# Optimization experiments

Hardware: AMD Instinct MI355X
Metric: run time of the kernel (lower is better)

The kernel has to match this reference:

```python
import jax, jax.numpy as jnp
import numpy as np

D, H, L, FF, EPS = 3, 3, 12, 2048, 1e-5
B, C, T = 32, 2, 64


def _ln(x, g, b):
    m = jnp.mean(x, -1, keepdims=True)
    v = jnp.mean((x - m) ** 2, -1, keepdims=True)
    return (x - m) / jnp.sqrt(v + EPS) * g + b


def _mha(xq, xkv, w, b, ow, ob):
    # xq: [Tq,B,D], xkv: [S,B,D]; w: [3D,D] packed q/k/v like torch in_proj_weight
    Tq, Bb, _ = xq.shape
    S = xkv.shape[0]
    q = xq @ w[:D].T + b[:D]
    k = xkv @ w[D:2 * D].T + b[D:2 * D]
    v = xkv @ w[2 * D:].T + b[2 * D:]
    dh = D // H  # = 1
    q = q.reshape(Tq, Bb, H, dh)
    k = k.reshape(S, Bb, H, dh)
    v = v.reshape(S, Bb, H, dh)
    scores = jnp.einsum('qbhd,kbhd->bhqk', q, k) * (1.0 / np.sqrt(dh))
    att = jax.nn.softmax(scores, axis=-1)
    o = jnp.einsum('bhqk,kbhd->qbhd', att, v).reshape(Tq, Bb, D)
    return o @ ow.T + ob


def _ffn(x, w1, b1, w2, b2):
    return jax.nn.relu(x @ w1.T + b1) @ w2.T + b2


def _encode(x, p):
    def layer(h, pl):
        aw, ab, aow, aob, g1, b1, g2, b2, f1w, f1b, f2w, f2b = pl
        h = _ln(h + _mha(h, h, aw, ab, aow, aob), g1, b1)
        h = _ln(h + _ffn(h, f1w, f1b, f2w, f2b), g2, b2)
        return h, None
    h, _ = jax.lax.scan(layer, x, p)
    return h


def _decode(tgt, mem, p):
    def layer(h, pl):
        (sw, sb, sow, sob, cw, cb, cow, cob,
         g1, b1, g2, b2, g3, b3, f1w, f1b, f2w, f2b) = pl
        h = _ln(h + _mha(h, h, sw, sb, sow, sob), g1, b1)      # self-attn (no mask, as in source)
        h = _ln(h + _mha(h, mem, cw, cb, cow, cob), g2, b2)    # cross-attn
        h = _ln(h + _ffn(h, f1w, f1b, f2w, f2b), g3, b3)
        return h, None
    h, _ = jax.lax.scan(layer, tgt, p)
    return h


def _forward(src, angle, enc_p, enc_ng, enc_nb, dec_p, dec_ng, dec_nb):
    Bb, _, Tt = src.shape
    a = jnp.broadcast_to(angle.reshape(Bb, 1, 1), (Bb, 1, Tt))
    x = jnp.transpose(jnp.concatenate([src, a], axis=1), (2, 0, 1))  # [T,B,3]
    mem = _ln(_encode(x, enc_p), enc_ng, enc_nb)  # encoder memory is loop-invariant

    def dec(o):
        return _ln(_decode(o, mem, dec_p), dec_ng, dec_nb)

    out = jnp.zeros_like(x).at[0].set(x[0])

    def step(o, t):
        pred = dec(o)
        return o.at[t].set(pred[t]), None

    out, _ = jax.lax.scan(step, out, jnp.arange(1, Tt))
    return jnp.transpose(out, (1, 2, 0))  # [B,3,T]


def setup_inputs() -> dict:
    key = jax.random.key(0)
    it = iter(jax.random.split(key, 40))
    def n(shape, s=0.05):
        return jax.random.normal(next(it), shape, dtype=jnp.float32) * s
    inp = {
        'src': jax.random.normal(next(it), (B, C, T), dtype=jnp.float32),
        'angle': jax.random.normal(next(it), (B,), dtype=jnp.float32),
        'enc_attn_w': n((L, 3 * D, D)), 'enc_attn_b': n((L, 3 * D)),
        'enc_attn_ow': n((L, D, D)), 'enc_attn_ob': n((L, D)),
        'enc_ln1_g': jnp.ones((L, D)), 'enc_ln1_b': jnp.zeros((L, D)),
        'enc_ln2_g': jnp.ones((L, D)), 'enc_ln2_b': jnp.zeros((L, D)),
        'enc_ff1_w': n((L, FF, D)), 'enc_ff1_b': n((L, FF)),
        'enc_ff2_w': n((L, D, FF)), 'enc_ff2_b': n((L, D)),
        'enc_norm_g': jnp.ones((D,)), 'enc_norm_b': jnp.zeros((D,)),
        'dec_sa_w': n((L, 3 * D, D)), 'dec_sa_b': n((L, 3 * D)),
        'dec_sa_ow': n((L, D, D)), 'dec_sa_ob': n((L, D)),
        'dec_ca_w': n((L, 3 * D, D)), 'dec_ca_b': n((L, 3 * D)),
        'dec_ca_ow': n((L, D, D)), 'dec_ca_ob': n((L, D)),
        'dec_ln1_g': jnp.ones((L, D)), 'dec_ln1_b': jnp.zeros((L, D)),
        'dec_ln2_g': jnp.ones((L, D)), 'dec_ln2_b': jnp.zeros((L, D)),
        'dec_ln3_g': jnp.ones((L, D)), 'dec_ln3_b': jnp.zeros((L, D)),
        'dec_ff1_w': n((L, FF, D)), 'dec_ff1_b': n((L, FF)),
        'dec_ff2_w': n((L, D, FF)), 'dec_ff2_b': n((L, D)),
        'dec_norm_g': jnp.ones((D,)), 'dec_norm_b': jnp.zeros((D,)),
    }
    return inp


def reference(src, angle,
              enc_attn_w, enc_attn_b, enc_attn_ow, enc_attn_ob,
              enc_ln1_g, enc_ln1_b, enc_ln2_g, enc_ln2_b,
              enc_ff1_w, enc_ff1_b, enc_ff2_w, enc_ff2_b,
              enc_norm_g, enc_norm_b,
              dec_sa_w, dec_sa_b, dec_sa_ow, dec_sa_ob,
              dec_ca_w, dec_ca_b, dec_ca_ow, dec_ca_ob,
              dec_ln1_g, dec_ln1_b, dec_ln2_g, dec_ln2_b, dec_ln3_g, dec_ln3_b,
              dec_ff1_w, dec_ff1_b, dec_ff2_w, dec_ff2_b,
              dec_norm_g, dec_norm_b):
    enc_p = (enc_attn_w, enc_attn_b, enc_attn_ow, enc_attn_ob,
             enc_ln1_g, enc_ln1_b, enc_ln2_g, enc_ln2_b,
             enc_ff1_w, enc_ff1_b, enc_ff2_w, enc_ff2_b)
    dec_p = (dec_sa_w, dec_sa_b, dec_sa_ow, dec_sa_ob,
             dec_ca_w, dec_ca_b, dec_ca_ow, dec_ca_ob,
             dec_ln1_g, dec_ln1_b, dec_ln2_g, dec_ln2_b, dec_ln3_g, dec_ln3_b,
             dec_ff1_w, dec_ff1_b, dec_ff2_w, dec_ff2_b)
    return _forward(src, angle, enc_p, enc_norm_g, enc_norm_b, dec_p, dec_norm_g, dec_norm_b)
```

## Files before the change

### kernel.cpp

```cpp
#include <hip/hip_runtime.h>

#define DEV static __device__ __forceinline__

typedef _Float16 h2 __attribute__((ext_vector_type(2)));

DEV float fdot2f(h2 a, h2 b, float c) {
#if __has_builtin(__builtin_amdgcn_fdot2)
  return __builtin_amdgcn_fdot2(a, b, c, false);
#else
  return c + (float)a.x * (float)b.x + (float)a.y * (float)b.y;
#endif
}

DEV void ln3(float& a, float& b, float& c, const float* g, const float* bt) {
  float m = (a + b + c) * (1.0f / 3.0f);
  float d0 = a - m, d1 = b - m, d2 = c - m;
  float v = (d0 * d0 + d1 * d1 + d2 * d2) * (1.0f / 3.0f);
  float rs = rsqrtf(v + 1e-5f);
  a = fmaf(d0 * rs, g[0], bt[0]);
  b = fmaf(d1 * rs, g[1], bt[1]);
  c = fmaf(d2 * rs, g[2], bt[2]);
}

DEV unsigned pkh2(float a, float b) {
  h2 v = {(_Float16)a, (_Float16)b};
  return __builtin_bit_cast(unsigned, v);
}

__global__ void __launch_bounds__(256) prepack_kernel(
    const float* ea_w, const float* ea_b, const float* ea_ow, const float* ea_ob,
    const float* el1g, const float* el1b, const float* el2g, const float* el2b,
    const float* ef1w, const float* ef1b, const float* ef2w, const float* ef2b,
    const float* eng, const float* enb,
    const float* dsw, const float* dsb, const float* dsow, const float* dsob,
    const float* dcw, const float* dcb, const float* dcow, const float* dcob,
    const float* dl1g, const float* dl1b, const float* dl2g, const float* dl2b,
    const float* dl3g, const float* dl3b,
    const float* df1w, const float* df1b, const float* df2w, const float* df2b,
    const float* dng, const float* dnb,
    float* ws) {
  const int l = blockIdx.x, tid = threadIdx.x;
  const bool enc = l < 12;
  const int li = enc ? l : l - 12;
  const float* f1w = (enc ? ef1w : df1w) + li * 2048 * 3;
  const float* f1b = (enc ? ef1b : df1b) + li * 2048;
  const float* f2w = (enc ? ef2w : df2w) + li * 3 * 2048;
  uint4* FA4 = (uint4*)ws + (size_t)l * 2048;
  uint4* FB4 = FA4 + 1024;
  for (int jp = tid; jp < 1024; jp += 256) {
    const int j0 = jp * 2, j1 = j0 + 1;
    uint4 A;
    A.x = pkh2(f1w[j0 * 3 + 0], f1w[j1 * 3 + 0]);
    A.y = pkh2(f1w[j0 * 3 + 1], f1w[j1 * 3 + 1]);
    A.z = pkh2(f1w[j0 * 3 + 2], f1w[j1 * 3 + 2]);
    A.w = pkh2(f1b[j0], f1b[j1]);
    FA4[jp] = A;
    uint4 Bv;
    Bv.x = pkh2(f2w[j0], f2w[j1]);
    Bv.y = pkh2(f2w[2048 + j0], f2w[2048 + j1]);
    Bv.z = pkh2(f2w[4096 + j0], f2w[4096 + j1]);
    Bv.w = 0u;
    FB4[jp] = Bv;
  }
  float* S = ws + 196608 + l * 128;
  if (tid == 0) {
    const float* aw = (enc ? ea_w : dsw) + li * 27;
    const float* ab = (enc ? ea_b : dsb) + li * 9;
    const float* aow = (enc ? ea_ow : dsow) + li * 9;
    const float* aob = (enc ? ea_ob : dsob) + li * 3;
    for (int i = 0; i < 27; ++i) S[i] = aw[i];
    for (int i = 0; i < 9; ++i) S[27 + i] = ab[i];
    for (int i = 0; i < 9; ++i) S[36 + i] = aow[i];
    for (int i = 0; i < 3; ++i) S[45 + i] = aob[i];
    const float* p;
    p = (enc ? el1g : dl1g) + li * 3; for (int i = 0; i < 3; ++i) S[48 + i] = p[i];
    p = (enc ? el1b : dl1b) + li * 3; for (int i = 0; i < 3; ++i) S[51 + i] = p[i];
    p = (enc ? el2g : dl2g) + li * 3; for (int i = 0; i < 3; ++i) S[54 + i] = p[i];
    p = (enc ? el2b : dl2b) + li * 3; for (int i = 0; i < 3; ++i) S[57 + i] = p[i];
    p = (enc ? ef2b : df2b) + li * 3; for (int i = 0; i < 3; ++i) S[60 + i] = p[i];
    if (!enc) {
      const float* cw = dcw + li * 27;
      for (int i = 0; i < 9; ++i) {
        S[64 + i] = cw[i];
        S[94 + i] = cw[9 + i];
        S[106 + i] = cw[18 + i];
      }
      const float* cb = dcb + li * 9;
      for (int i = 0; i < 3; ++i) {
        S[73 + i] = cb[i];
        S[103 + i] = cb[3 + i];
        S[115 + i] = cb[6 + i];
      }
      for (int i = 0; i < 9; ++i) S[76 + i] = dcow[li * 9 + i];
      for (int i = 0; i < 3; ++i) S[85 + i] = dcob[li * 3 + i];
      p = dl3g + li * 3; for (int i = 0; i < 3; ++i) S[88 + i] = p[i];
      p = dl3b + li * 3; for (int i = 0; i < 3; ++i) S[91 + i] = p[i];
    }
  }
  if (l == 0 && tid == 1) {
    float* G = ws + 196608 + 24 * 128;
    for (int i = 0; i < 3; ++i) {
      G[i] = eng[i]; G[3 + i] = enb[i];
      G[6 + i] = dng[i]; G[9 + i] = dnb[i];
    }
  }
}

template <int NR>
DEV void ffn_core(const uint4* FA, uint4 pa0, uint4 pc0, uint4 pa1, uint4 pc1,
                  const float (&X0)[4], const float (&X1)[4], const float (&X2)[4],
                  float (&acc)[4][3], int lane) {
  h2 xd0[NR], xd1[NR], xd2[NR];
#pragma unroll
  for (int i = 0; i < NR; ++i) {
    xd0[i] = h2{(_Float16)X0[i], (_Float16)X0[i]};
    xd1[i] = h2{(_Float16)X1[i], (_Float16)X1[i]};
    xd2[i] = h2{(_Float16)X2[i], (_Float16)X2[i]};
  }
#pragma unroll
  for (int i = 0; i < NR; ++i) { acc[i][0] = 0.f; acc[i][1] = 0.f; acc[i][2] = 0.f; }
  const h2 z = {(_Float16)0, (_Float16)0};
  auto step = [&](uint4 a, uint4 c) {
    h2 wa0 = __builtin_bit_cast(h2, a.x), wa1 = __builtin_bit_cast(h2, a.y);
    h2 wa2 = __builtin_bit_cast(h2, a.z), bb = __builtin_bit_cast(h2, a.w);
    h2 wc0 = __builtin_bit_cast(h2, c.x), wc1 = __builtin_bit_cast(h2, c.y);
    h2 wc2 = __builtin_bit_cast(h2, c.z);
#pragma unroll
    for (int i = 0; i < NR; ++i) {
      h2 t = wa0 * xd0[i] + wa1 * xd1[i] + wa2 * xd2[i] + bb;
      t = __builtin_elementwise_max(t, z);
      acc[i][0] = fdot2f(wc0, t, acc[i][0]);
      acc[i][1] = fdot2f(wc1, t, acc[i][1]);
      acc[i][2] = fdot2f(wc2, t, acc[i][2]);
    }
  };
  step(pa0, pc0);
  step(pa1, pc1);
#pragma unroll 4
  for (int kk = 2; kk < 16; ++kk) {
    const int jp = lane + (kk << 6);
    step(FA[jp], FA[1024 + jp]);
  }
#pragma unroll
  for (int m = 1; m < 64; m <<= 1) {
#pragma unroll
    for (int i = 0; i < NR; ++i) {
      acc[i][0] += __shfl_xor(acc[i][0], m, 64);
      acc[i][1] += __shfl_xor(acc[i][1], m, 64);
      acc[i][2] += __shfl_xor(acc[i][2], m, 64);
    }
  }
}

template <bool DEC>
DEV void run_layer(const float* sm, const float* smn, const uint4* FA,
                   const float (*ckv)[8],
                   float (*h)[5], float (*hln)[5], float* kvq,
                   float (*p1)[25], float (*p2)[25],
                   float (*o_s)[5], const float* glob,
                   int R, int t, bool do_p1, bool from_os, bool wpred,
                   int wave, int lane, int tid) {
  uint4 pa0 = FA[lane], pc0 = FA[1024 + lane];
  uint4 pa1 = FA[64 + lane], pc1 = FA[1024 + 64 + lane];
  if (do_p1) {
    const int r = tid >> 4, o = tid & 15;
    if (r < R && o <= 9) {
      float x0, x1, x2;
      if (DEC && from_os) {
        const bool real = r < t;
        x0 = real ? o_s[r][0] : 0.f;
        x1 = real ? o_s[r][1] : 0.f;
        x2 = real ? o_s[r][2] : 0.f;
      } else {
        x0 = h[r][0]; x1 = h[r][1]; x2 = h[r][2];
      }
      if (o < 9) {
        float v = fmaf(sm[o * 3], x0,
                  fmaf(sm[o * 3 + 1], x1, fmaf(sm[o * 3 + 2], x2, sm[27 + o])));
        kvq[r * 13 + o + o / 3] = v;
      } else {
        kvq[r * 13 + 7] = (DEC && r == R - 1 && t > 0) ? (float)(64 - t) : 1.0f;
        if (DEC && from_os) { h[r][0] = x0; h[r][1] = x1; h[r][2] = x2; }
      }
    }
    if (DEC && o == 9 && r >= R) kvq[r * 13 + 7] = 0.f;
    __syncthreads();
  }
  if (wave < 12) {
    const int hd = wave % 3, c = wave / 3;
    const int p0 = c * 16;
    float den = 0.f, num = 0.f;
    if (p0 < R) {
      const float q = kvq[lane * 13 + hd] * 1.44269504f;
#pragma unroll
      for (int pp = 0; pp < 16; ++pp) {
        const int p = p0 + pp;
        float e = exp2f(q * kvq[p * 13 + 4 + hd]);
        if (DEC) e *= kvq[p * 13 + 7];
        den += e;
        num = fmaf(e, kvq[p * 13 + 8 + hd], num);
      }
    }
    p1[lane][2 * wave] = den;
    p1[lane][2 * wave + 1] = num;
  }
  __syncthreads();
  if (DEC) {
    if (wave < 12) {
      const int r = lane, hd = wave % 3, c = wave / 3;
      float d0 = p1[r][0] + p1[r][6] + p1[r][12] + p1[r][18];
      float n0 = p1[r][1] + p1[r][7] + p1[r][13] + p1[r][19];
      float d1 = p1[r][2] + p1[r][8] + p1[r][14] + p1[r][20];
      float n1 = p1[r][3] + p1[r][9] + p1[r][15] + p1[r][21];
      float d2 = p1[r][4] + p1[r][10] + p1[r][16] + p1[r][22];
      float n2 = p1[r][5] + p1[r][11] + p1[r][17] + p1[r][23];
      float oh0 = __fdividef(n0, d0), oh1 = __fdividef(n1, d1), oh2 = __fdividef(n2, d2);
      float a0 = fmaf(sm[36], oh0, fmaf(sm[37], oh1, fmaf(sm[38], oh2, sm[45]))) + h[r][0];
      float a1 = fmaf(sm[39], oh0, fmaf(sm[40], oh1, fmaf(sm[41], oh2, sm[46]))) + h[r][1];
      float a2 = fmaf(sm[42], oh0, fmaf(sm[43], oh1, fmaf(sm[44], oh2, sm[47]))) + h[r][2];
      ln3(a0, a1, a2, sm + 48, sm + 51);
      if (wave == 0 && r < R) { hln[r][0] = a0; hln[r][1] = a1; hln[r][2] = a2; }
      float q = fmaf(sm[64 + hd * 3], a0,
                fmaf(sm[64 + hd * 3 + 1], a1,
                fmaf(sm[64 + hd * 3 + 2], a2, sm[73 + hd]))) * 1.44269504f;
      const int p0 = c * 16;
      float den = 0.f, num = 0.f;
#pragma unroll
      for (int pp = 0; pp < 16; ++pp) {
        const int p = p0 + pp;
        float e = exp2f(q * ckv[p][hd]);
        den += e;
        num = fmaf(e, ckv[p][3 + hd], num);
      }
      p2[r][2 * wave] = den;
      p2[r][2 * wave + 1] = num;
    }
    __syncthreads();
  }
  {
    const int nr = (wave < R) ? (1 + (R - 1 - wave) / 16) : 0;
    if (nr > 0) {
      const float(*pp)[25] = DEC ? p2 : p1;
      const float* ow = DEC ? sm + 76 : sm + 36;
      const float* ob = DEC ? sm + 85 : sm + 45;
      const float* lg = DEC ? sm + 54 : sm + 48;
      const float* lb = DEC ? sm + 57 : sm + 51;
      float X0[4], X1[4], X2[4];
#pragma unroll
      for (int i = 0; i < 4; ++i) {
        X0[i] = 0.f; X1[i] = 0.f; X2[i] = 0.f;
        if (i < nr) {
          const int rc = wave + 16 * i;
          float d0 = pp[rc][0] + pp[rc][6] + pp[rc][12] + pp[rc][18];
          float n0 = pp[rc][1] + pp[rc][7] + pp[rc][13] + pp[rc][19];
          float d1 = pp[rc][2] + pp[rc][8] + pp[rc][14] + pp[rc][20];
          float n1 = pp[rc][3] + pp[rc][9] + pp[rc][15] + pp[rc][21];
          float d2 = pp[rc][4] + pp[rc][10] + pp[rc][16] + pp[rc][22];
          float n2 = pp[rc][5] + pp[rc][11] + pp[rc][17] + pp[rc][23];
          float oh0 = __fdividef(n0, d0), oh1 = __fdividef(n1, d1), oh2 = __fdividef(n2, d2);
          float hr0, hr1, hr2;
          if (DEC) { hr0 = hln[rc][0]; hr1 = hln[rc][1]; hr2 = hln[rc][2]; }
          else     { hr0 = h[rc][0];   hr1 = h[rc][1];   hr2 = h[rc][2]; }
          float a0 = fmaf(ow[0], oh0, fmaf(ow[1], oh1, fmaf(ow[2], oh2, ob[0]))) + hr0;
          float a1 = fmaf(ow[3], oh0, fmaf(ow[4], oh1, fmaf(ow[5], oh2, ob[1]))) + hr1;
          float a2 = fmaf(ow[6], oh0, fmaf(ow[7], oh1, fmaf(ow[8], oh2, ob[2]))) + hr2;
          ln3(a0, a1, a2, lg, lb);
          X0[i] = a0; X1[i] = a1; X2[i] = a2;
        }
      }
      float acc[4][3];
      switch (nr) {
        case 1: ffn_core<1>(FA, pa0, pc0, pa1, pc1, X0, X1, X2, acc, lane); break;
        case 2: ffn_core<2>(FA, pa0, pc0, pa1, pc1, X0, X1, X2, acc, lane); break;
        case 3: ffn_core<3>(FA, pa0, pc0, pa1, pc1, X0, X1, X2, acc, lane); break;
        default: ffn_core<4>(FA, pa0, pc0, pa1, pc1, X0, X1, X2, acc, lane); break;
      }
      const float* fg = DEC ? sm + 88 : sm + 54;
      const float* fb = DEC ? sm + 91 : sm + 57;
#pragma unroll
      for (int i = 0; i < 4; ++i) {
        if (i < nr) {
          const int r = wave + 16 * i;
          float y0 = acc[i][0] + sm[60] + X0[i];
          float y1 = acc[i][1] + sm[61] + X1[i];
          float y2 = acc[i][2] + sm[62] + X2[i];
          ln3(y0, y1, y2, fg, fb);
          if (lane == 0) {
            h[r][0] = y0; h[r][1] = y1; h[r][2] = y2;
            if (DEC && wpred && r == R - 1) {
              float z0 = y0, z1 = y1, z2 = y2;
              ln3(z0, z1, z2, glob + 6, glob + 9);
              o_s[t][0] = z0; o_s[t][1] = z1; o_s[t][2] = z2;
            }
          }
          if (smn && lane >= 9 * i && lane < 9 * i + 9) {
            const int o = lane - 9 * i;
            kvq[r * 13 + o + o / 3] =
                fmaf(smn[o * 3], y0,
                fmaf(smn[o * 3 + 1], y1, fmaf(smn[o * 3 + 2], y2, smn[27 + o])));
          }
        }
      }
    }
    __syncthreads();
  }
}

__global__ void __launch_bounds__(1024) tf_kernel(const float* src, const float* angle,
                                                  const float* ws, float* out) {
  __shared__ float small_s[24][128];
  __shared__ float glob[16];
  __shared__ float h[64][5];
  __shared__ float hln[64][5];
  __shared__ float kvq[64 * 13];
  __shared__ float p1[64][25];
  __shared__ float p2[64][25];
  __shared__ float o_s[64][5];
  __shared__ float ckcv[12][64][8];
  const int b = blockIdx.x;
  const int tid = threadIdx.x, wave = tid >> 6, lane = tid & 63;
  const uint4* FABg = (const uint4*)ws;
  const float* SM = ws + 196608;
  const float* GB = SM + 24 * 128;
  for (int i = tid; i < 24 * 128; i += 1024) ((float*)small_s)[i] = SM[i];
  if (tid < 16) glob[tid] = GB[tid];
  if (tid < 64) {
    float x0 = src[b * 128 + tid];
    float x1 = src[b * 128 + 64 + tid];
    float x2 = angle[b];
    h[tid][0] = x0; h[tid][1] = x1; h[tid][2] = x2;
    o_s[tid][0] = (tid == 0) ? x0 : 0.f;
    o_s[tid][1] = (tid == 0) ? x1 : 0.f;
    o_s[tid][2] = (tid == 0) ? x2 : 0.f;
  }
  __syncthreads();
  for (int l = 0; l < 12; ++l)
    run_layer<false>(small_s[l], (l < 11) ? small_s[l + 1] : nullptr,
                     FABg + (size_t)l * 2048, nullptr,
                     h, hln, kvq, p1, p2, o_s, glob,
                     64, 0, l == 0, false, false, wave, lane, tid);
  if (tid < 64) {
    float a = h[tid][0], bb = h[tid][1], c = h[tid][2];
    ln3(a, bb, c, glob + 0, glob + 3);
    h[tid][0] = a; h[tid][1] = bb; h[tid][2] = c;
  }
  __syncthreads();
  if (wave < 12) {
    const float* sm = small_s[12 + wave];
    float m0 = h[lane][0], m1 = h[lane][1], m2 = h[lane][2];
    float k0 = fmaf(sm[94], m0, fmaf(sm[95], m1, fmaf(sm[96], m2, sm[103])));
    float k1 = fmaf(sm[97], m0, fmaf(sm[98], m1, fmaf(sm[99], m2, sm[104])));
    float k2 = fmaf(sm[100], m0, fmaf(sm[101], m1, fmaf(sm[102], m2, sm[105])));
    float v0 = fmaf(sm[106], m0, fmaf(sm[107], m1, fmaf(sm[108], m2, sm[115])));
    float v1 = fmaf(sm[109], m0, fmaf(sm[110], m1, fmaf(sm[111], m2, sm[116])));
    float v2 = fmaf(sm[112], m0, fmaf(sm[113], m1, fmaf(sm[114], m2, sm[117])));
    ckcv[wave][lane][0] = k0; ckcv[wave][lane][1] = k1; ckcv[wave][lane][2] = k2;
    ckcv[wave][lane][3] = v0; ckcv[wave][lane][4] = v1; ckcv[wave][lane][5] = v2;
  }
  __syncthreads();
  for (int t = 1; t < 64; ++t) {
    const int R = t + 1;
    for (int li = 0; li < 12; ++li)
      run_layer<true>(small_s[12 + li], (li < 11) ? small_s[12 + li + 1] : nullptr,
                      FABg + (size_t)(12 + li) * 2048,
                      (const float(*)[8])ckcv[li],
                      h, hln, kvq, p1, p2, o_s, glob, R, t,
                      li == 0, li == 0, li == 11,
                      wave, lane, tid);
  }
  if (tid < 192) {
    int d = tid / 64, tt = tid % 64;
    out[b * 192 + tid] = o_s[tt][d];
  }
}

extern "C" void kernel_launch(void* const* d_in, const int* in_sizes, int n_in,
                              void* d_out, int out_size, void* d_ws, size_t ws_size,
                              hipStream_t stream) {
  (void)in_sizes; (void)n_in; (void)out_size; (void)ws_size;
  float* ws = (float*)d_ws;
  prepack_kernel<<<24, 256, 0, stream>>>(
      (const float*)d_in[2], (const float*)d_in[3], (const float*)d_in[4], (const float*)d_in[5],
      (const float*)d_in[6], (const float*)d_in[7], (const float*)d_in[8], (const float*)d_in[9],
      (const float*)d_in[10], (const float*)d_in[11], (const float*)d_in[12], (const float*)d_in[13],
      (const float*)d_in[14], (const float*)d_in[15],
      (const float*)d_in[16], (const float*)d_in[17], (const float*)d_in[18], (const float*)d_in[19],
      (const float*)d_in[20], (const float*)d_in[21], (const float*)d_in[22], (const float*)d_in[23],
      (const float*)d_in[24], (const float*)d_in[25], (const float*)d_in[26], (const float*)d_in[27],
      (const float*)d_in[28], (const float*)d_in[29],
      (const float*)d_in[30], (const float*)d_in[31], (const float*)d_in[32], (const float*)d_in[33],
      (const float*)d_in[34], (const float*)d_in[35],
      ws);
  tf_kernel<<<32, 1024, 0, stream>>>((const float*)d_in[0], (const float*)d_in[1], ws,
                                     (float*)d_out);
}
```

Baseline: 6.544 ms.

## Fuse attention, cross-attention and FFN per layer into one barrier phase

New measurement: 6.638 ms. About the same (+1.4%).

```diff
diff --git a/kernel.cpp b/kernel.cpp
--- a/kernel.cpp
+++ b/kernel.cpp
@@ -127,11 +127,11 @@
     h2 wc2 = __builtin_bit_cast(h2, c.z);
 #pragma unroll
     for (int i = 0; i < NR; ++i) {
-      h2 t = wa0 * xd0[i] + wa1 * xd1[i] + wa2 * xd2[i] + bb;
-      t = __builtin_elementwise_max(t, z);
-      acc[i][0] = fdot2f(wc0, t, acc[i][0]);
-      acc[i][1] = fdot2f(wc1, t, acc[i][1]);
-      acc[i][2] = fdot2f(wc2, t, acc[i][2]);
+      h2 tt = wa0 * xd0[i] + wa1 * xd1[i] + wa2 * xd2[i] + bb;
+      tt = __builtin_elementwise_max(tt, z);
+      acc[i][0] = fdot2f(wc0, tt, acc[i][0]);
+      acc[i][1] = fdot2f(wc1, tt, acc[i][1]);
+      acc[i][2] = fdot2f(wc2, tt, acc[i][2]);
     }
   };
   step(pa0, pc0);
@@ -152,171 +152,162 @@
   }
 }
 
+DEV void qkv_phase(const float* sm, float* kvw, const float4* src4,
+                   bool from_os, int R, int t, int tid) {
+  const int r = tid >> 4, o = tid & 15;
+  if (r < R && o < 9) {
+    float4 xv = src4[r];
+    float x0 = xv.x, x1 = xv.y, x2 = xv.z;
+    if (from_os && r >= t) { x0 = 0.f; x1 = 0.f; x2 = 0.f; }
+    kvw[r * 13 + o + o / 3] =
+        fmaf(sm[o * 3], x0, fmaf(sm[o * 3 + 1], x1, fmaf(sm[o * 3 + 2], x2, sm[27 + o])));
+  }
+}
+
 template <bool DEC>
-DEV void run_layer(const float* sm, const float* smn, const uint4* FA,
-                   const float (*ckv)[8],
-                   float (*h)[5], float (*hln)[5], float* kvq,
-                   float (*p1)[25], float (*p2)[25],
-                   float (*o_s)[5], const float* glob,
-                   int R, int t, bool do_p1, bool from_os, bool wpred,
-                   int wave, int lane, int tid) {
+DEV void run_fused(const float* sm, const float* smn, const uint4* FA,
+                   const float* ckv, const float* kvr, float* kvw,
+                   float4* o_s4, float4* h4, const float* glob,
+                   float (&hall)[4][3],
+                   int R, int t, bool wpred, bool seed,
+                   int wave, int lane) {
   uint4 pa0 = FA[lane], pc0 = FA[1024 + lane];
-  uint4 pa1 = FA[64 + lane], pc1 = FA[1024 + 64 + lane];
-  if (do_p1) {
-    const int r = tid >> 4, o = tid & 15;
-    if (r < R && o <= 9) {
-      float x0, x1, x2;
-      if (DEC && from_os) {
+  uint4 pa1 = FA[64 + lane], pc1 = FA[1088 + lane];
+  const int g = lane & 15, ig = lane >> 4;
+  const int arow = wave + 16 * ig;
+  if (seed) {
+    if (DEC) {
+#pragma unroll
+      for (int i = 0; i < 4; ++i) {
+        const int r = wave + 16 * i;
+        float4 xv = o_s4[r];
         const bool real = r < t;
-        x0 = real ? o_s[r][0] : 0.f;
-        x1 = real ? o_s[r][1] : 0.f;
-        x2 = real ? o_s[r][2] : 0.f;
-      } else {
-        x0 = h[r][0]; x1 = h[r][1]; x2 = h[r][2];
-      }
-      if (o < 9) {
-        float v = fmaf(sm[o * 3], x0,
-                  fmaf(sm[o * 3 + 1], x1, fmaf(sm[o * 3 + 2], x2, sm[27 + o])));
-        kvq[r * 13 + o + o / 3] = v;
-      } else {
-        kvq[r * 13 + 7] = (DEC && r == R - 1 && t > 0) ? (float)(64 - t) : 1.0f;
-        if (DEC && from_os) { h[r][0] = x0; h[r][1] = x1; h[r][2] = x2; }
-      }
-    }
-    if (DEC && o == 9 && r >= R) kvq[r * 13 + 7] = 0.f;
-    __syncthreads();
-  }
-  if (wave < 12) {
-    const int hd = wave % 3, c = wave / 3;
-    const int p0 = c * 16;
-    float den = 0.f, num = 0.f;
-    if (p0 < R) {
-      const float q = kvq[lane * 13 + hd] * 1.44269504f;
+        hall[i][0] = real ? xv.x : 0.f;
+        hall[i][1] = real ? xv.y : 0.f;
+        hall[i][2] = real ? xv.z : 0.f;
+      }
+    } else {
+#pragma unroll
+      for (int i = 0; i < 4; ++i) {
+        float4 xv = h4[wave + 16 * i];
+        hall[i][0] = xv.x; hall[i][1] = xv.y; hall[i][2] = xv.z;
+      }
+    }
+  }
+  float hr0 = hall[0][0], hr1 = hall[0][1], hr2 = hall[0][2];
+  if (ig == 1) { hr0 = hall[1][0]; hr1 = hall[1][1]; hr2 = hall[1][2]; }
+  else if (ig == 2) { hr0 = hall[2][0]; hr1 = hall[2][1]; hr2 = hall[2][2]; }
+  else if (ig == 3) { hr0 = hall[3][0]; hr1 = hall[3][1]; hr2 = hall[3][2]; }
+  const int hd = g % 3, ch = g / 3;
+  float den = 0.f, num = 0.f;
+  if (g < 12) {
+    const float q = kvr[arow * 13 + hd] * 1.44269504f;
+#pragma unroll
+    for (int pp = 0; pp < 16; ++pp) {
+      const int p = ch * 16 + pp;
+      float e = exp2f(q * kvr[p * 13 + 4 + hd]);
+      if (DEC) {
+        e = (p > t) ? 0.f : e;
+        e = (p == t) ? e * (float)(64 - t) : e;
+      }
+      den += e;
+      num = fmaf(e, kvr[p * 13 + 8 + hd], num);
+    }
+  }
+  float dd = den + __shfl_down(den, 6, 64); dd += __shfl_down(dd, 3, 64);
+  float nn = num + __shfl_down(num, 6, 64); nn += __shfl_down(nn, 3, 64);
+  const float oh = __fdividef(nn, dd);
+  const int base = lane & 48;
+  const float oh0 = __shfl(oh, base, 64);
+  const float oh1 = __shfl(oh, base + 1, 64);
+  const float oh2 = __shfl(oh, base + 2, 64);
+  float a0 = fmaf(sm[36], oh0, fmaf(sm[37], oh1, fmaf(sm[38], oh2, sm[45]))) + hr0;
+  float a1 = fmaf(sm[39], oh0, fmaf(sm[40], oh1, fmaf(sm[41], oh2, sm[46]))) + hr1;
+  float a2 = fmaf(sm[42], oh0, fmaf(sm[43], oh1, fmaf(sm[44], oh2, sm[47]))) + hr2;
+  ln3(a0, a1, a2, sm + 48, sm + 51);
+  float x0, x1, x2;
+  if (DEC) {
+    float dc = 0.f, nc = 0.f;
+    if (g < 12) {
+      const float qc = fmaf(sm[64 + hd * 3], a0,
+                       fmaf(sm[64 + hd * 3 + 1], a1,
+                       fmaf(sm[64 + hd * 3 + 2], a2, sm[73 + hd]))) * 1.44269504f;
 #pragma unroll
       for (int pp = 0; pp < 16; ++pp) {
-        const int p = p0 + pp;
-        float e = exp2f(q * kvq[p * 13 + 4 + hd]);
-        if (DEC) e *= kvq[p * 13 + 7];
-        den += e;
-        num = fmaf(e, kvq[p * 13 + 8 + hd], num);
-      }
-    }
-    p1[lane][2 * wave] = den;
-    p1[lane][2 * wave + 1] = num;
-  }
-  __syncthreads();
-  if (DEC) {
-    if (wave < 12) {
-      const int r = lane, hd = wave % 3, c = wave / 3;
-      float d0 = p1[r][0] + p1[r][6] + p1[r][12] + p1[r][18];
-      float n0 = p1[r][1] + p1[r][7] + p1[r][13] + p1[r][19];
-      float d1 = p1[r][2] + p1[r][8] + p1[r][14] + p1[r][20];
-      float n1 = p1[r][3] + p1[r][9] + p1[r][15] + p1[r][21];
-      float d2 = p1[r][4] + p1[r][10] + p1[r][16] + p1[r][22];
-      float n2 = p1[r][5] + p1[r][11] + p1[r][17] + p1[r][23];
-      float oh0 = __fdividef(n0, d0), oh1 = __fdividef(n1, d1), oh2 = __fdividef(n2, d2);
-      float a0 = fmaf(sm[36], oh0, fmaf(sm[37], oh1, fmaf(sm[38], oh2, sm[45]))) + h[r][0];
-      float a1 = fmaf(sm[39], oh0, fmaf(sm[40], oh1, fmaf(sm[41], oh2, sm[46]))) + h[r][1];
-      float a2 = fmaf(sm[42], oh0, fmaf(sm[43], oh1, fmaf(sm[44], oh2, sm[47]))) + h[r][2];
-      ln3(a0, a1, a2, sm + 48, sm + 51);
-      if (wave == 0 && r < R) { hln[r][0] = a0; hln[r][1] = a1; hln[r][2] = a2; }
-      float q = fmaf(sm[64 + hd * 3], a0,
-                fmaf(sm[64 + hd * 3 + 1], a1,
-                fmaf(sm[64 + hd * 3 + 2], a2, sm[73 + hd]))) * 1.44269504f;
-      const int p0 = c * 16;
-      float den = 0.f, num = 0.f;
-#pragma unroll
-      for (int pp = 0; pp < 16; ++pp) {
-        const int p = p0 + pp;
-        float e = exp2f(q * ckv[p][hd]);
-        den += e;
-        num = fmaf(e, ckv[p][3 + hd], num);
-      }
-      p2[r][2 * wave] = den;
-      p2[r][2 * wave + 1] = num;
-    }
-    __syncthreads();
-  }
-  {
-    const int nr = (wave < R) ? (1 + (R - 1 - wave) / 16) : 0;
-    if (nr > 0) {
-      const float(*pp)[25] = DEC ? p2 : p1;
-      const float* ow = DEC ? sm + 76 : sm + 36;
-      const float* ob = DEC ? sm + 85 : sm + 45;
-      const float* lg = DEC ? sm + 54 : sm + 48;
-      const float* lb = DEC ? sm + 57 : sm + 51;
-      float X0[4], X1[4], X2[4];
-#pragma unroll
-      for (int i = 0; i < 4; ++i) {
-        X0[i] = 0.f; X1[i] = 0.f; X2[i] = 0.f;
-        if (i < nr) {
-          const int rc = wave + 16 * i;
-          float d0 = pp[rc][0] + pp[rc][6] + pp[rc][12] + pp[rc][18];
-          float n0 = pp[rc][1] + pp[rc][7] + pp[rc][13] + pp[rc][19];
-          float d1 = pp[rc][2] + pp[rc][8] + pp[rc][14] + pp[rc][20];
-          float n1 = pp[rc][3] + pp[rc][9] + pp[rc][15] + pp[rc][21];
-          float d2 = pp[rc][4] + pp[rc][10] + pp[rc][16] + pp[rc][22];
-          float n2 = pp[rc][5] + pp[rc][11] + pp[rc][17] + pp[rc][23];
-          float oh0 = __fdividef(n0, d0), oh1 = __fdividef(n1, d1), oh2 = __fdividef(n2, d2);
-          float hr0, hr1, hr2;
-          if (DEC) { hr0 = hln[rc][0]; hr1 = hln[rc][1]; hr2 = hln[rc][2]; }
-          else     { hr0 = h[rc][0];   hr1 = h[rc][1];   hr2 = h[rc][2]; }
-          float a0 = fmaf(ow[0], oh0, fmaf(ow[1], oh1, fmaf(ow[2], oh2, ob[0]))) + hr0;
-          float a1 = fmaf(ow[3], oh0, fmaf(ow[4], oh1, fmaf(ow[5], oh2, ob[1]))) + hr1;
-          float a2 = fmaf(ow[6], oh0, fmaf(ow[7], oh1, fmaf(ow[8], oh2, ob[2]))) + hr2;
-          ln3(a0, a1, a2, lg, lb);
-          X0[i] = a0; X1[i] = a1; X2[i] = a2;
-        }
-      }
-      float acc[4][3];
-      switch (nr) {
-        case 1: ffn_core<1>(FA, pa0, pc0, pa1, pc1, X0, X1, X2, acc, lane); break;
-        case 2: ffn_core<2>(FA, pa0, pc0, pa1, pc1, X0, X1, X2, acc, lane); break;
-        case 3: ffn_core<3>(FA, pa0, pc0, pa1, pc1, X0, X1, X2, acc, lane); break;
-        default: ffn_core<4>(FA, pa0, pc0, pa1, pc1, X0, X1, X2, acc, lane); break;
-      }
-      const float* fg = DEC ? sm + 88 : sm + 54;
-      const float* fb = DEC ? sm + 91 : sm + 57;
-#pragma unroll
-      for (int i = 0; i < 4; ++i) {
-        if (i < nr) {
-          const int r = wave + 16 * i;
-          float y0 = acc[i][0] + sm[60] + X0[i];
-          float y1 = acc[i][1] + sm[61] + X1[i];
-          float y2 = acc[i][2] + sm[62] + X2[i];
-          ln3(y0, y1, y2, fg, fb);
-          if (lane == 0) {
-            h[r][0] = y0; h[r][1] = y1; h[r][2] = y2;
-            if (DEC && wpred && r == R - 1) {
-              float z0 = y0, z1 = y1, z2 = y2;
-              ln3(z0, z1, z2, glob + 6, glob + 9);
-              o_s[t][0] = z0; o_s[t][1] = z1; o_s[t][2] = z2;
-            }
-          }
-          if (smn && lane >= 9 * i && lane < 9 * i + 9) {
-            const int o = lane - 9 * i;
-            kvq[r * 13 + o + o / 3] =
-                fmaf(smn[o * 3], y0,
-                fmaf(smn[o * 3 + 1], y1, fmaf(smn[o * 3 + 2], y2, smn[27 + o])));
+        const int p = ch * 16 + pp;
+        float e = exp2f(qc * ckv[p * 13 + 4 + hd]);
+        dc += e;
+        nc = fmaf(e, ckv[p * 13 + 8 + hd], nc);
+      }
+    }
+    float dd2 = dc + __shfl_down(dc, 6, 64); dd2 += __shfl_down(dd2, 3, 64);
+    float nn2 = nc + __shfl_down(nc, 6, 64); nn2 += __shfl_down(nn2, 3, 64);
+    const float ohc = __fdividef(nn2, dd2);
+    const float c0 = __shfl(ohc, base, 64);
+    const float c1 = __shfl(ohc, base + 1, 64);
+    const float c2 = __shfl(ohc, base + 2, 64);
+    x0 = fmaf(sm[76], c0, fmaf(sm[77], c1, fmaf(sm[78], c2, sm[85]))) + a0;
+    x1 = fmaf(sm[79], c0, fmaf(sm[80], c1, fmaf(sm[81], c2, sm[86]))) + a1;
+    x2 = fmaf(sm[82], c0, fmaf(sm[83], c1, fmaf(sm[84], c2, sm[87]))) + a2;
+    ln3(x0, x1, x2, sm + 54, sm + 57);
+  } else {
+    x0 = a0; x1 = a1; x2 = a2;
+  }
+  float X0[4], X1[4], X2[4];
+#pragma unroll
+  for (int i = 0; i < 4; ++i) {
+    X0[i] = __shfl(x0, 16 * i, 64);
+    X1[i] = __shfl(x1, 16 * i, 64);
+    X2[i] = __shfl(x2, 16 * i, 64);
+  }
+  const int nr = (wave < R) ? (1 + (R - 1 - wave) / 16) : 0;
+  if (nr > 0) {
+    float acc[4][3];
+    switch (nr) {
+      case 1: ffn_core<1>(FA, pa0, pc0, pa1, pc1, X0, X1, X2, acc, lane); break;
+      case 2: ffn_core<2>(FA, pa0, pc0, pa1, pc1, X0, X1, X2, acc, lane); break;
+      case 3: ffn_core<3>(FA, pa0, pc0, pa1, pc1, X0, X1, X2, acc, lane); break;
+      default: ffn_core<4>(FA, pa0, pc0, pa1, pc1, X0, X1, X2, acc, lane); break;
+    }
+    const float* fg = DEC ? sm + 88 : sm + 54;
+    const float* fb = DEC ? sm + 91 : sm + 57;
+#pragma unroll
+    for (int i = 0; i < 4; ++i) {
+      if (i < nr) {
+        const int r = wave + 16 * i;
+        float y0 = acc[i][0] + sm[60] + X0[i];
+        float y1 = acc[i][1] + sm[61] + X1[i];
+        float y2 = acc[i][2] + sm[62] + X2[i];
+        ln3(y0, y1, y2, fg, fb);
+        hall[i][0] = y0; hall[i][1] = y1; hall[i][2] = y2;
+        if (lane == 0) {
+          if (!DEC) h4[r] = float4{y0, y1, y2, 0.f};
+          if (DEC && wpred && r == R - 1) {
+            float z0 = y0, z1 = y1, z2 = y2;
+            ln3(z0, z1, z2, glob + 6, glob + 9);
+            o_s4[t] = float4{z0, z1, z2, 0.f};
           }
         }
-      }
-    }
-    __syncthreads();
-  }
+        if (smn && lane >= 9 * i && lane < 9 * i + 9) {
+          const int o = lane - 9 * i;
+          kvw[r * 13 + o + o / 3] =
+              fmaf(smn[o * 3], y0,
+              fmaf(smn[o * 3 + 1], y1, fmaf(smn[o * 3 + 2], y2, smn[27 + o])));
+        }
+      }
+    }
+  }
+  __syncthreads();
 }
 
 __global__ void __launch_bounds__(1024) tf_kernel(const float* src, const float* angle,
                                                   const float* ws, float* out) {
   __shared__ float small_s[24][128];
   __shared__ float glob[16];
-  __shared__ float h[64][5];
-  __shared__ float hln[64][5];
-  __shared__ float kvq[64 * 13];
-  __shared__ float p1[64][25];
-  __shared__ float p2[64][25];
-  __shared__ float o_s[64][5];
-  __shared__ float ckcv[12][64][8];
+  __shared__ float kv[2][832];
+  __shared__ __align__(16) float4 o_s4[64];
+  __shared__ __align__(16) float4 h4[64];
+  __shared__ float ckv13[12][832];
   const int b = blockIdx.x;
   const int tid = threadIdx.x, wave = tid >> 6, lane = tid & 63;
   const uint4* FABg = (const uint4*)ws;
@@ -328,49 +319,56 @@
     float x0 = src[b * 128 + tid];
     float x1 = src[b * 128 + 64 + tid];
     float x2 = angle[b];
-    h[tid][0] = x0; h[tid][1] = x1; h[tid][2] = x2;
-    o_s[tid][0] = (tid == 0) ? x0 : 0.f;
-    o_s[tid][1] = (tid == 0) ? x1 : 0.f;
-    o_s[tid][2] = (tid == 0) ? x2 : 0.f;
-  }
+    h4[tid] = float4{x0, x1, x2, 0.f};
+    o_s4[tid] = (tid == 0) ? float4{x0, x1, x2, 0.f} : float4{0.f, 0.f, 0.f, 0.f};
+  }
+  __syncthreads();
+  float hall[4][3];
+  qkv_phase(small_s[0], kv[0], h4, false, 64, 0, tid);
   __syncthreads();
   for (int l = 0; l < 12; ++l)
-    run_layer<false>(small_s[l], (l < 11) ? small_s[l + 1] : nullptr,
+    run_fused<false>(small_s[l], (l < 11) ? small_s[l + 1] : nullptr,
                      FABg + (size_t)l * 2048, nullptr,
-                     h, hln, kvq, p1, p2, o_s, glob,
-                     64, 0, l == 0, false, false, wave, lane, tid);
+                     kv[l & 1], kv[(l + 1) & 1],
+                     o_s4, h4, glob, hall, 64, 0, false, l == 0,
+                     wave, lane);
   if (tid < 64) {
-    float a = h[tid][0], bb = h[tid][1], c = h[tid][2];
+    float4 hx = h4[tid];
+    float a = hx.x, bb = hx.y, c = hx.z;
     ln3(a, bb, c, glob + 0, glob + 3);
-    h[tid][0] = a; h[tid][1] = bb; h[tid][2] = c;
+    h4[tid] = float4{a, bb, c, 0.f};
   }
   __syncthreads();
   if (wave < 12) {
     const float* sm = small_s[12 + wave];
-    float m0 = h[lane][0], m1 = h[lane][1], m2 = h[lane][2];
-    float k0 = fmaf(sm[94], m0, fmaf(sm[95], m1, fmaf(sm[96], m2, sm[103])));
-    float k1 = fmaf(sm[97], m0, fmaf(sm[98], m1, fmaf(sm[99], m2, sm[104])));
-    float k2 = fmaf(sm[100], m0, fmaf(sm[101], m1, fmaf(sm[102], m2, sm[105])));
-    float v0 = fmaf(sm[106], m0, fmaf(sm[107], m1, fmaf(sm[108], m2, sm[115])));
-    float v1 = fmaf(sm[109], m0, fmaf(sm[110], m1, fmaf(sm[111], m2, sm[116])));
-    float v2 = fmaf(sm[112], m0, fmaf(sm[113], m1, fmaf(sm[114], m2, sm[117])));
-    ckcv[wave][lane][0] = k0; ckcv[wave][lane][1] = k1; ckcv[wave][lane][2] = k2;
-    ckcv[wave][lane][3] = v0; ckcv[wave][lane][4] = v1; ckcv[wave][lane][5] = v2;
+    float4 hx = h4[lane];
+#pragma unroll
+    for (int hdd = 0; hdd < 3; ++hdd) {
+      float k = fmaf(sm[94 + hdd * 3], hx.x,
+                fmaf(sm[94 + hdd * 3 + 1], hx.y,
+                fmaf(sm[94 + hdd * 3 + 2], hx.z, sm[103 + hdd])));
+      float v = fmaf(sm[106 + hdd * 3], hx.x,
+                fmaf(sm[106 + hdd * 3 + 1], hx.y,
+                fmaf(sm[106 + hdd * 3 + 2], hx.z, sm[115 + hdd])));
+      ckv13[wave][lane * 13 + 4 + hdd] = k;
+      ckv13[wave][lane * 13 + 8 + hdd] = v;
+    }
   }
   __syncthreads();
   for (int t = 1; t < 64; ++t) {
     const int R = t + 1;
+    qkv_phase(small_s[12], kv[0], o_s4, true, R, t, tid);
+    __syncthreads();
     for (int li = 0; li < 12; ++li)
-      run_layer<true>(small_s[12 + li], (li < 11) ? small_s[12 + li + 1] : nullptr,
-                      FABg + (size_t)(12 + li) * 2048,
-                      (const float(*)[8])ckcv[li],
-                      h, hln, kvq, p1, p2, o_s, glob, R, t,
-                      li == 0, li == 0, li == 11,
-                      wave, lane, tid);
+      run_fused<true>(small_s[12 + li], (li < 11) ? small_s[13 + li] : nullptr,
+                      FABg + (size_t)(12 + li) * 2048, ckv13[li],
+                      kv[li & 1], kv[(li + 1) & 1],
+                      o_s4, nullptr, glob, hall, R, t,
+                      li == 11, li == 0, wave, lane);
   }
   if (tid < 192) {
     int d = tid / 64, tt = tid % 64;
-    out[b * 192 + tid] = o_s[tt][d];
+    out[b * 192 + tid] = ((const float*)o_s4)[tt * 4 + d];
   }
 }
 
```
